# Optimization experiments

Measured on AMD Instinct MI355X. Metric: run time of the kernel, lower is better.

Reference implementation:

```python
import jax, jax.numpy as jnp
import numpy as np

B, U1, U2 = 4, 2048, 2048
C = 256      # in_feat_dim
F = 256      # feat_dim
M = 4        # num_modes
D = C // M   # attention_mode_dim = 64
ATTN_CLIP = 500.0
LN_EPS = 1e-12


def setup_inputs() -> dict:
    key = jax.random.key(0)
    ks = jax.random.split(key, 8)
    s = 0.02  # base_initializer_range
    inp = {
        "query_feat": jax.random.normal(ks[0], (B, U1, C), jnp.float32),
        "key_feat": jax.random.normal(ks[1], (B, U2, C), jnp.float32),
        "Wq": jax.random.normal(ks[2], (M * D, C), jnp.float32) * s,
        "bq": jnp.zeros((M * D,), jnp.float32),
    }
    # tie_qk_scheme='shared': key linear shares query weights
    inp["Wk"] = inp["Wq"]
    inp["bk"] = inp["bq"]
    inp["Wv"] = jax.random.normal(ks[3], (M * F, C), jnp.float32) * s  # first_linear, v_has_bias=False
    inp["W_mid"] = jax.random.normal(ks[4], (F, F), jnp.float32) * s   # MMSharedMid shared_linear
    inp["b_mid"] = jnp.zeros((F,), jnp.float32)
    inp["W_out"] = jax.random.normal(ks[5], (M, F, F), jnp.float32) * s  # grouped 1x1 conv, per mode
    inp["b_out"] = jnp.zeros((M, F), jnp.float32)
    inp["ln_g"] = jnp.ones((F,), jnp.float32)   # resout LayerNorm
    inp["ln_b"] = jnp.zeros((F,), jnp.float32)
    inp["W_score"] = jax.random.normal(ks[6], (1, F), jnp.float32) * s  # LearnedSoftAggregate
    inp["b_score"] = jnp.zeros((1,), jnp.float32)
    return inp


def _layer_norm(x, g, b):
    mu = jnp.mean(x, axis=-1, keepdims=True)
    var = jnp.var(x, axis=-1, keepdims=True)
    return (x - mu) * jax.lax.rsqrt(var + LN_EPS) * g + b


def reference(query_feat, key_feat, Wq, bq, Wk, bk, Wv, W_mid, b_mid,
              W_out, b_out, ln_g, ln_b, W_score, b_score):
    # --- tied-QK multi-mode attention ---
    q = (query_feat @ Wq.T + bq).reshape(B, U1, M, D)
    k = (key_feat @ Wk.T + bk).reshape(B, U2, M, D)
    scores = jnp.einsum('bimd,bjmd->bmij', q, k) / jnp.sqrt(jnp.float32(D))
    scores = jnp.clip(scores, -ATTN_CLIP, ATTN_CLIP)  # attn_clip
    probs = jax.nn.softmax(scores, axis=-1)           # [B, M, U1, U2]

    # --- ExpandedFeatTrans: value projection + fusion ---
    v = (key_feat @ Wv.T).reshape(B, U2, M, F)        # first_linear (no bias)
    fused = jnp.einsum('bmij,bjmf->bmif', probs, v)   # [B, M, U1, F]

    # MMSharedMid: shared linear over F + gelu (dropout = identity in eval)
    mid = jax.nn.gelu(fused @ W_mid.T + b_mid, approximate=False)

    # MMPrivateOutput: per-mode grouped 1x1 conv; NOTE the original code computes
    # x_comb = x + shortcut but then layer-norms x (shortcut dropped) - kept faithful.
    out = jnp.einsum('bmif,mgf->bmig', mid, W_out) + b_out[None, :, None, :]
    out = _layer_norm(out, ln_g, ln_b)                # [B, M, U1, F]

    # LearnedSoftAggregate over modes (group_dim=1, keepdim=False)
    mode_scores = out @ W_score.T + b_score           # [B, M, U1, 1]
    mode_probs = jax.nn.softmax(mode_scores, axis=1)
    return jnp.sum(out * mode_probs, axis=1)          # [B, U1, F]
```

## Files before the change

kernel.cpp:

```cpp
#include <hip/hip_runtime.h>

typedef __attribute__((ext_vector_type(8))) short short8;
typedef __attribute__((ext_vector_type(4))) float f32x4;
typedef __attribute__((ext_vector_type(16))) float f32x16;
typedef unsigned short u16t;
typedef unsigned int u32t;

#define MFMA16(a, b, c) __builtin_amdgcn_mfma_f32_16x16x32_bf16((a), (b), (c), 0, 0, 0)
#define MFMA32(a, b, c) __builtin_amdgcn_mfma_f32_32x32x16_bf16((a), (b), (c), 0, 0, 0)

__device__ __forceinline__ u16t f2bf(float f) {
  u32t u = __float_as_uint(f);
  u32t r = u + 0x7fffu + ((u >> 16) & 1u);
  return (u16t)(r >> 16);
}
__device__ __forceinline__ float bf2f(u16t b) {
  return __uint_as_float(((u32t)b) << 16);
}
__device__ __forceinline__ short8 pack8(float4 a0, float4 a1) {
  short8 r;
  r[0] = (short)f2bf(a0.x); r[1] = (short)f2bf(a0.y);
  r[2] = (short)f2bf(a0.z); r[3] = (short)f2bf(a0.w);
  r[4] = (short)f2bf(a1.x); r[5] = (short)f2bf(a1.y);
  r[6] = (short)f2bf(a1.z); r[7] = (short)f2bf(a1.w);
  return r;
}
__device__ __forceinline__ u32t packrhu(float a, float b) {
  u32t ua = __float_as_uint(a) + 0x8000u;
  u32t ub = __float_as_uint(b) + 0x8000u;
  return (ua >> 16) | (ub & 0xffff0000u);
}

__global__ __launch_bounds__(256) void cvt_kernel(
    const float* __restrict__ Wq, const float* __restrict__ Wv,
    const float* __restrict__ Wm, const float* __restrict__ Wo,
    u16t* __restrict__ WqB, u16t* __restrict__ WvB,
    u16t* __restrict__ WmB, u16t* __restrict__ WoB) {
  const int blk = blockIdx.x, tid = threadIdx.x;
  const float* src; u16t* dst; int base;
  if (blk < 64)       { src = Wq; dst = WqB; base = blk * 1024; }
  else if (blk < 320) { src = Wv; dst = WvB; base = (blk - 64) * 1024; }
  else if (blk < 384) { src = Wm; dst = WmB; base = (blk - 320) * 1024; }
  else                { src = Wo; dst = WoB; base = (blk - 384) * 1024; }
  int i = base + tid * 4;
  float4 v = *(const float4*)(src + i);
  ushort4 o;
  o.x = f2bf(v.x); o.y = f2bf(v.y); o.z = f2bf(v.z); o.w = f2bf(v.w);
  *(ushort4*)(dst + i) = o;
}

__global__ __launch_bounds__(256, 4) void proj_kernel(
    const float* __restrict__ query, const float* __restrict__ key,
    const u16t* __restrict__ WqB, const u16t* __restrict__ WvB,
    const float* __restrict__ bq,
    u16t* __restrict__ QfB, u16t* __restrict__ KfB, u16t* __restrict__ VfB) {
  __shared__ __align__(16) u16t Cs[64 * 72];
  const int tid = threadIdx.x;
  const int w = tid >> 6, lane = tid & 63, quad = lane >> 4, l15 = lane & 15;
  const int l31 = lane & 31, h8 = (lane >> 5) * 8;
  const int wrow = (w >> 1) * 32, wcol = (w & 1) * 32;

  const float* A; const u16t* W16; const float* bias;
  float ascale; u16t* out; int mode, bx, byg;
  const int blk = blockIdx.x;
  if (blk < 128) {
    A = query; W16 = WqB; bias = bq; ascale = 0.125f; out = QfB; mode = 0; bx = blk; byg = 0;
  } else if (blk < 256) {
    A = key; W16 = WqB; bias = bq; ascale = 1.0f; out = KfB; mode = 0; bx = blk - 128; byg = 0;
  } else {
    int v2 = blk - 256;
    A = key; W16 = WvB; bias = nullptr; ascale = 1.0f; out = VfB; mode = 1;
    bx = v2 & 127; byg = v2 >> 7;
  }
  const int rt = bx * 64;

  const f32x4 fz = {0.f, 0.f, 0.f, 0.f};
  f32x4 acc[4][2][2];
#pragma unroll
  for (int n = 0; n < 4; n++)
#pragma unroll
    for (int i = 0; i < 2; i++)
#pragma unroll
      for (int j = 0; j < 2; j++) acc[n][i][j] = fz;

  const float* arow0 = A + (size_t)(rt + wrow + l15) * 256;
  const float* arow1 = A + (size_t)(rt + wrow + 16 + l15) * 256;
  const u16t* wbase = W16 + (size_t)(byg * 256 + wcol + l15) * 256;

#pragma unroll
  for (int ks = 0; ks < 8; ++ks) {
    const int kk = ks * 32 + quad * 8;
    float4 a00 = *(const float4*)(arow0 + kk);
    float4 a01 = *(const float4*)(arow0 + kk + 4);
    float4 a10 = *(const float4*)(arow1 + kk);
    float4 a11 = *(const float4*)(arow1 + kk + 4);
    a00.x *= ascale; a00.y *= ascale; a00.z *= ascale; a00.w *= ascale;
    a01.x *= ascale; a01.y *= ascale; a01.z *= ascale; a01.w *= ascale;
    a10.x *= ascale; a10.y *= ascale; a10.z *= ascale; a10.w *= ascale;
    a11.x *= ascale; a11.y *= ascale; a11.z *= ascale; a11.w *= ascale;
    short8 af0 = pack8(a00, a01);
    short8 af1 = pack8(a10, a11);
#pragma unroll
    for (int nby = 0; nby < 4; ++nby) {
      const u16t* wb = wbase + (size_t)nby * 64 * 256 + kk;
      short8 bw0 = *(const short8*)(wb);
      short8 bw1 = *(const short8*)(wb + 16 * 256);
      acc[nby][0][0] = MFMA16(af0, bw0, acc[nby][0][0]);
      acc[nby][0][1] = MFMA16(af0, bw1, acc[nby][0][1]);
      acc[nby][1][0] = MFMA16(af1, bw0, acc[nby][1][0]);
      acc[nby][1][1] = MFMA16(af1, bw1, acc[nby][1][1]);
    }
  }

#pragma unroll 1
  for (int nby = 0; nby < 4; ++nby) {
    const int by = byg * 4 + nby;
    const int ct = by * 64;
    __syncthreads();
    if (mode == 0) {
#pragma unroll
      for (int i = 0; i < 2; i++) {
        int rl = wrow + i * 16 + quad * 4;
#pragma unroll
        for (int j = 0; j < 2; j++) {
          int cl = wcol + j * 16 + l15;
          float bv = bias ? bias[ct + cl] * ascale : 0.f;
#pragma unroll
          for (int rg = 0; rg < 4; ++rg)
            Cs[(rl + rg) * 72 + cl] = f2bf(acc[nby][i][j][rg] + bv);
        }
      }
    } else {
#pragma unroll
      for (int i = 0; i < 2; i++) {
        int rl = wrow + i * 16 + quad * 4;
#pragma unroll
        for (int j = 0; j < 2; j++) {
          int cl = wcol + j * 16 + l15;
          ushort4 pk;
          pk.x = f2bf(acc[nby][i][j][0]);
          pk.y = f2bf(acc[nby][i][j][1]);
          pk.z = f2bf(acc[nby][i][j][2]);
          pk.w = f2bf(acc[nby][i][j][3]);
          *(ushort4*)&Cs[cl * 72 + rl] = pk;
        }
      }
    }
    __syncthreads();
#pragma unroll
    for (int t2 = 0; t2 < 2; ++t2) {
      short8 frag = *(const short8*)&Cs[(t2 * 32 + l31) * 72 + w * 16 + h8];
      size_t base;
      if (mode == 0) {
        int b = rt >> 11, m = by;
        int it32 = ((rt & 2047) >> 5) + t2;
        base = (((size_t)(b * 4 + m) * 64 + it32) * 4 + w) * 512;
      } else {
        int b = rt >> 11, m = by >> 2;
        int fb = ((by & 3) << 1) + t2;
        int jt16 = ((rt & 2047) >> 4) + w;
        base = (((size_t)(b * 4 + m) * 8 + fb) * 128 + jt16) * 512;
      }
      *(short8*)(out + base + lane * 8) = frag;
    }
  }
}

__global__ __launch_bounds__(256, 4) void attn_kernel(
    const u16t* __restrict__ Qf, const u16t* __restrict__ Kf,
    const u16t* __restrict__ Vf,
    const u16t* __restrict__ Wmid, const u16t* __restrict__ Wout,
    const float* __restrict__ b_mid, const float* __restrict__ b_out,
    const float* __restrict__ ln_g, const float* __restrict__ ln_b,
    const float* __restrict__ Wsc, const float* __restrict__ b_sc,
    u16t* __restrict__ out_ln, float* __restrict__ scoresWS) {
  __shared__ __align__(16) u16t smF[32 * 264];
  __shared__ __align__(16) u16t smP[2][32 * 132];
  __shared__ float smL[128];
  __shared__ float smR[128];
  __shared__ float smS[64];
  const int tid = threadIdx.x;
  const int w = tid >> 6, lane = tid & 63, quad = lane >> 4, l15 = lane & 15;
  const int l31 = lane & 31, h = lane >> 5;
  const int L = blockIdx.x;
  const int xcd = L & 7, slot = L >> 3;
  const int bm = xcd * 2 + (slot >> 6);
  const int it32 = slot & 63;
  const int m = bm & 3;
  const int q0 = it32 * 32;

  const size_t lane8 = (size_t)lane * 8;

  const u16t* qbase = Qf + ((size_t)(bm * 64 + it32) * 4) * 512 + lane8;
  short8 qf4[4];
#pragma unroll
  for (int ksd = 0; ksd < 4; ++ksd)
    qf4[ksd] = *(const short8*)(qbase + ksd * 512);

  const u16t* kbase = Kf + ((size_t)bm * 256) * 512 + lane8;
  const u16t* vbase = Vf + ((size_t)(bm * 8 + 2 * w) * 128) * 512 + lane8;

  f32x16 facc[2];
#pragma unroll
  for (int j = 0; j < 2; j++)
#pragma unroll
    for (int r = 0; r < 16; r++) facc[j][r] = 0.f;
  float lsum = 0.f;

  short8 kf4[4];
#pragma unroll
  for (int ksd = 0; ksd < 4; ++ksd)
    kf4[ksd] = *(const short8*)(kbase + (size_t)w * 2048 + ksd * 512);

  {
    f32x16 sacc;
#pragma unroll
    for (int r = 0; r < 16; r++) sacc[r] = 0.f;
#pragma unroll
    for (int ksd = 0; ksd < 4; ++ksd)
      sacc = MFMA32(kf4[ksd], qf4[ksd], sacc);
    float ls = 0.f;
#pragma unroll
    for (int tt = 0; tt < 8; ++tt) {
      const int jl = ((2 * tt) & 3) + 8 * ((2 * tt) >> 2) + 4 * h;
      float p0 = __expf(sacc[2 * tt]);
      float p1 = __expf(sacc[2 * tt + 1]);
      ls += p0 + p1;
      *(u32t*)&smP[0][l31 * 132 + w * 32 + jl] = packrhu(p0, p1);
    }
    lsum += ls;
  }
#pragma unroll
  for (int ksd = 0; ksd < 4; ++ksd)
    kf4[ksd] = *(const short8*)(kbase + (size_t)(4 + w) * 2048 + ksd * 512);
  __syncthreads();

#pragma unroll 1
  for (int t = 0; t < 16; ++t) {
    u16t* Pb = &smP[t & 1][0];
    u16t* Pn = &smP[(t + 1) & 1][0];

    if (t < 15) {
      f32x16 sacc;
#pragma unroll
      for (int r = 0; r < 16; r++) sacc[r] = 0.f;
#pragma unroll
      for (int ksd = 0; ksd < 4; ++ksd)
        sacc = MFMA32(kf4[ksd], qf4[ksd], sacc);
      float ls = 0.f;
#pragma unroll
      for (int tt = 0; tt < 8; ++tt) {
        const int jl = ((2 * tt) & 3) + 8 * ((2 * tt) >> 2) + 4 * h;
        float p0 = __expf(sacc[2 * tt]);
        float p1 = __expf(sacc[2 * tt + 1]);
        ls += p0 + p1;
        *(u32t*)&Pn[l31 * 132 + w * 32 + jl] = packrhu(p0, p1);
      }
      lsum += ls;
    }
    if (t < 14) {
      const int jn = (t + 2) * 4 + w;
#pragma unroll
      for (int ksd = 0; ksd < 4; ++ksd)
        kf4[ksd] = *(const short8*)(kbase + (size_t)jn * 2048 + ksd * 512);
    }
#pragma unroll
    for (int jj = 0; jj < 4; ++jj) {
      short8 vf[2][2];
#pragma unroll
      for (int fb = 0; fb < 2; ++fb)
#pragma unroll
        for (int ks2 = 0; ks2 < 2; ++ks2)
          vf[fb][ks2] = *(const short8*)(vbase + ((size_t)fb * 128 + (t * 8 + jj * 2 + ks2)) * 512);
      short8 bbL[2];
#pragma unroll
      for (int ks2 = 0; ks2 < 2; ++ks2)
        bbL[ks2] = *(const short8*)&Pb[l31 * 132 + jj * 32 + ks2 * 16 + h * 8];
      facc[0] = MFMA32(vf[0][0], bbL[0], facc[0]);
      facc[0] = MFMA32(vf[0][1], bbL[1], facc[0]);
      facc[1] = MFMA32(vf[1][0], bbL[0], facc[1]);
      facc[1] = MFMA32(vf[1][1], bbL[1], facc[1]);
    }
    __syncthreads();
  }

  lsum += __shfl_xor(lsum, 32);
  if (h == 0) smL[w * 32 + l31] = lsum;
  __syncthreads();
  float inv = 1.f / (smL[l31] + smL[32 + l31] + smL[64 + l31] + smL[96 + l31]);

#pragma unroll
  for (int fb = 0; fb < 2; ++fb) {
#pragma unroll
    for (int g = 0; g < 4; ++g) {
      int fbase = w * 64 + fb * 32 + 8 * g + 4 * h;
      ushort4 pk4;
      pk4.x = f2bf(facc[fb][4 * g + 0] * inv);
      pk4.y = f2bf(facc[fb][4 * g + 1] * inv);
      pk4.z = f2bf(facc[fb][4 * g + 2] * inv);
      pk4.w = f2bf(facc[fb][4 * g + 3] * inv);
      *(ushort4*)&smF[l31 * 264 + fbase] = pk4;
    }
  }
  __syncthreads();

  const int rgrp = w >> 1, ch = w & 1;
  const int rowq = rgrp * 16 + quad * 4;
  const f32x4 fz4 = {0.f, 0.f, 0.f, 0.f};

  f32x4 macc[8];
#pragma unroll
  for (int i = 0; i < 8; i++) macc[i] = fz4;
  for (int kc = 0; kc < 8; ++kc) {
    short8 af = *(const short8*)&smF[(rgrp * 16 + l15) * 264 + kc * 32 + quad * 8];
#pragma unroll
    for (int nb = 0; nb < 8; ++nb) {
      short8 bw = *(const short8*)(Wmid + (size_t)(ch * 128 + nb * 16 + l15) * 256 + kc * 32 + quad * 8);
      macc[nb] = MFMA16(af, bw, macc[nb]);
    }
  }
#pragma unroll
  for (int nb = 0; nb < 8; ++nb) {
    int c = ch * 128 + nb * 16 + l15;
    float bmv = b_mid[c];
#pragma unroll
    for (int rg = 0; rg < 4; ++rg) {
      float x = macc[nb][rg] + bmv;
      macc[nb][rg] = 0.5f * x * (1.f + erff(x * 0.70710678118654752f));
    }
  }
  __syncthreads();
#pragma unroll
  for (int nb = 0; nb < 8; ++nb)
#pragma unroll
    for (int rg = 0; rg < 4; ++rg)
      smF[(rowq + rg) * 264 + ch * 128 + nb * 16 + l15] = f2bf(macc[nb][rg]);
  __syncthreads();

  const u16t* Wo = Wout + (size_t)m * 65536;
  f32x4 oacc[8];
#pragma unroll
  for (int i = 0; i < 8; i++) oacc[i] = fz4;
  for (int kc = 0; kc < 8; ++kc) {
    short8 af = *(const short8*)&smF[(rgrp * 16 + l15) * 264 + kc * 32 + quad * 8];
#pragma unroll
    for (int nb = 0; nb < 8; ++nb) {
      short8 bw = *(const short8*)(Wo + (size_t)(ch * 128 + nb * 16 + l15) * 256 + kc * 32 + quad * 8);
      oacc[nb] = MFMA16(af, bw, oacc[nb]);
    }
  }

  float sum[4] = {0, 0, 0, 0}, sq[4] = {0, 0, 0, 0};
#pragma unroll
  for (int nb = 0; nb < 8; ++nb) {
    int c = ch * 128 + nb * 16 + l15;
    float bo = b_out[m * 256 + c];
#pragma unroll
    for (int rg = 0; rg < 4; ++rg) {
      float x = oacc[nb][rg] + bo;
      oacc[nb][rg] = x;
      sum[rg] += x;
      sq[rg] += x * x;
    }
  }
#pragma unroll
  for (int rg = 0; rg < 4; ++rg) {
    float s = sum[rg], s2 = sq[rg];
    s += __shfl_xor(s, 1); s += __shfl_xor(s, 2); s += __shfl_xor(s, 4); s += __shfl_xor(s, 8);
    s2 += __shfl_xor(s2, 1); s2 += __shfl_xor(s2, 2); s2 += __shfl_xor(s2, 4); s2 += __shfl_xor(s2, 8);
    if (l15 == 0) {
      smR[(rowq + rg) + 32 * ch] = s;
      smR[64 + (rowq + rg) + 32 * ch] = s2;
    }
  }
  __syncthreads();
  float mu[4], rstd[4];
#pragma unroll
  for (int rg = 0; rg < 4; ++rg) {
    int r = rowq + rg;
    float s = smR[r] + smR[r + 32];
    float s2 = smR[64 + r] + smR[64 + r + 32];
    float mean = s * (1.f / 256.f);
    float var = s2 * (1.f / 256.f) - mean * mean;
    mu[rg] = mean;
    rstd[rg] = rsqrtf(var + 1e-12f);
  }

  float scp[4] = {0, 0, 0, 0};
#pragma unroll
  for (int nb = 0; nb < 8; ++nb) {
    int c = ch * 128 + nb * 16 + l15;
    float g = ln_g[c], bb2 = ln_b[c], wsv = Wsc[c];
#pragma unroll
    for (int rg = 0; rg < 4; ++rg) {
      float xn = (oacc[nb][rg] - mu[rg]) * rstd[rg] * g + bb2;
      out_ln[((size_t)bm * 2048 + (q0 + rowq + rg)) * 256 + c] = f2bf(xn);
      scp[rg] += xn * wsv;
    }
  }
#pragma unroll
  for (int rg = 0; rg < 4; ++rg) {
    float s = scp[rg];
    s += __shfl_xor(s, 1); s += __shfl_xor(s, 2); s += __shfl_xor(s, 4); s += __shfl_xor(s, 8);
    if (l15 == 0) smS[(rowq + rg) + 32 * ch] = s;
  }
  __syncthreads();
  if (ch == 0 && l15 == 0) {
#pragma unroll
    for (int rg = 0; rg < 4; ++rg) {
      int r = rowq + rg;
      scoresWS[bm * 2048 + q0 + r] = smS[r] + smS[r + 32] + b_sc[0];
    }
  }
}

__global__ __launch_bounds__(256) void agg_kernel(
    const u16t* __restrict__ out_ln, const float* __restrict__ scoresWS,
    float* __restrict__ out) {
  const int row = blockIdx.x;
  const int c = threadIdx.x;
  const int b = row >> 11, i = row & 2047;
  float s0 = scoresWS[(b * 4 + 0) * 2048 + i];
  float s1 = scoresWS[(b * 4 + 1) * 2048 + i];
  float s2 = scoresWS[(b * 4 + 2) * 2048 + i];
  float s3 = scoresWS[(b * 4 + 3) * 2048 + i];
  float mx = fmaxf(fmaxf(s0, s1), fmaxf(s2, s3));
  float e0 = __expf(s0 - mx), e1 = __expf(s1 - mx), e2 = __expf(s2 - mx), e3 = __expf(s3 - mx);
  float inv = 1.f / (e0 + e1 + e2 + e3);
  float acc = e0 * inv * bf2f(out_ln[((size_t)(b * 4 + 0) * 2048 + i) * 256 + c]) +
              e1 * inv * bf2f(out_ln[((size_t)(b * 4 + 1) * 2048 + i) * 256 + c]) +
              e2 * inv * bf2f(out_ln[((size_t)(b * 4 + 2) * 2048 + i) * 256 + c]) +
              e3 * inv * bf2f(out_ln[((size_t)(b * 4 + 3) * 2048 + i) * 256 + c]);
  out[(size_t)row * 256 + c] = acc;
}

extern "C" void kernel_launch(void* const* d_in, const int* in_sizes, int n_in,
                              void* d_out, int out_size, void* d_ws, size_t ws_size,
                              hipStream_t stream) {
  (void)in_sizes; (void)n_in; (void)out_size; (void)ws_size;
  const float* query = (const float*)d_in[0];
  const float* key   = (const float*)d_in[1];
  const float* Wq    = (const float*)d_in[2];
  const float* bq    = (const float*)d_in[3];
  const float* Wv    = (const float*)d_in[6];
  const float* Wm    = (const float*)d_in[7];
  const float* bmid  = (const float*)d_in[8];
  const float* Wo    = (const float*)d_in[9];
  const float* bo    = (const float*)d_in[10];
  const float* lng   = (const float*)d_in[11];
  const float* lnb   = (const float*)d_in[12];
  const float* Wsc   = (const float*)d_in[13];
  const float* bsc   = (const float*)d_in[14];

  char* p = (char*)d_ws;
  u16t* QfB = (u16t*)p; p += (size_t)2097152 * 2;
  u16t* KfB = (u16t*)p; p += (size_t)2097152 * 2;
  u16t* VfB = (u16t*)p; p += (size_t)8388608 * 2;
  u16t* WmB = (u16t*)p; p += (size_t)65536 * 2;
  u16t* WoB = (u16t*)p; p += (size_t)262144 * 2;
  u16t* WqB = (u16t*)p; p += (size_t)65536 * 2;
  u16t* WvB = (u16t*)p; p += (size_t)262144 * 2;
  u16t* outLn = (u16t*)p; p += (size_t)8388608 * 2;
  float* scWS = (float*)p; p += (size_t)32768 * 4;

  cvt_kernel<<<640, 256, 0, stream>>>(Wq, Wv, Wm, Wo, WqB, WvB, WmB, WoB);

  proj_kernel<<<768, 256, 0, stream>>>(query, key, WqB, WvB, bq,
                                       QfB, KfB, VfB);

  attn_kernel<<<1024, 256, 0, stream>>>(QfB, KfB, VfB, WmB, WoB,
                                        bmid, bo, lng, lnb, Wsc, bsc,
                                        outLn, scWS);

  agg_kernel<<<8192, 256, 0, stream>>>(outLn, scWS, (float*)d_out);
}
```

Before: 277.7 us.

## Reuse key A-fragments across K and V tiles; prefetch V fragments in attention

The projection kernel now loads and converts each 64-row block of the input once into register fragments. It then loops over several output column tiles, K and V together for key blocks, which halves the grid and avoids re-reading and re-packing key_feat for the separate K and V blocks. In the attention kernel, all 16 V fragments for a tile are issued as loads at the top of each iteration, ahead of the score MFMAs, so their latency overlaps compute. The occupancy hint is lowered to 3 waves per SIMD to make room for the extra registers. The trade-offs are more registers per thread, lower occupancy, and fewer, longer-running projection blocks.

```diff
diff --git a/kernel.cpp b/kernel.cpp
--- a/kernel.cpp
+++ b/kernel.cpp
@@ -49,7 +49,7 @@
   *(ushort4*)(dst + i) = o;
 }
 
-__global__ __launch_bounds__(256, 4) void proj_kernel(
+__global__ __launch_bounds__(256) void proj_kernel(
     const float* __restrict__ query, const float* __restrict__ key,
     const u16t* __restrict__ WqB, const u16t* __restrict__ WvB,
     const float* __restrict__ bq,
@@ -60,62 +60,69 @@
   const int l31 = lane & 31, h8 = (lane >> 5) * 8;
   const int wrow = (w >> 1) * 32, wcol = (w & 1) * 32;
 
-  const float* A; const u16t* W16; const float* bias;
-  float ascale; u16t* out; int mode, bx, byg;
   const int blk = blockIdx.x;
+  const float* A; float ascale; int bx, nK, nV, kby0, vby0;
+  u16t* out0;
   if (blk < 128) {
-    A = query; W16 = WqB; bias = bq; ascale = 0.125f; out = QfB; mode = 0; bx = blk; byg = 0;
-  } else if (blk < 256) {
-    A = key; W16 = WqB; bias = bq; ascale = 1.0f; out = KfB; mode = 0; bx = blk - 128; byg = 0;
+    A = query; ascale = 0.125f; bx = blk; nK = 4; nV = 0; kby0 = 0; vby0 = 0;
+    out0 = QfB;
   } else {
-    int v2 = blk - 256;
-    A = key; W16 = WvB; bias = nullptr; ascale = 1.0f; out = VfB; mode = 1;
-    bx = v2 & 127; byg = v2 >> 7;
+    int kb = blk - 128;
+    bx = kb & 127; int byg = kb >> 7;
+    A = key; ascale = 1.0f; nK = 2; nV = 8; kby0 = byg * 2; vby0 = byg * 8;
+    out0 = KfB;
   }
   const int rt = bx * 64;
 
-  const f32x4 fz = {0.f, 0.f, 0.f, 0.f};
-  f32x4 acc[4][2][2];
-#pragma unroll
-  for (int n = 0; n < 4; n++)
+  short8 af[8][2];
+  {
+    const float* arow0 = A + (size_t)(rt + wrow + l15) * 256;
+    const float* arow1 = arow0 + 16 * 256;
+#pragma unroll
+    for (int ks = 0; ks < 8; ++ks) {
+      const int kk = ks * 32 + quad * 8;
+      float4 a00 = *(const float4*)(arow0 + kk);
+      float4 a01 = *(const float4*)(arow0 + kk + 4);
+      float4 a10 = *(const float4*)(arow1 + kk);
+      float4 a11 = *(const float4*)(arow1 + kk + 4);
+      a00.x *= ascale; a00.y *= ascale; a00.z *= ascale; a00.w *= ascale;
+      a01.x *= ascale; a01.y *= ascale; a01.z *= ascale; a01.w *= ascale;
+      a10.x *= ascale; a10.y *= ascale; a10.z *= ascale; a10.w *= ascale;
+      a11.x *= ascale; a11.y *= ascale; a11.z *= ascale; a11.w *= ascale;
+      af[ks][0] = pack8(a00, a01);
+      af[ks][1] = pack8(a10, a11);
+    }
+  }
+
+  const int ntiles = nK + nV;
+#pragma unroll 1
+  for (int tix = 0; tix < ntiles; ++tix) {
+    const bool isK = tix < nK;
+    const int by = isK ? (kby0 + tix) : (vby0 + (tix - nK));
+    const u16t* W16 = isK ? WqB : WvB;
+    u16t* outp = isK ? out0 : VfB;
+    const int mode = isK ? 0 : 1;
+    const int ct = by * 64;
+
+    const f32x4 fz = {0.f, 0.f, 0.f, 0.f};
+    f32x4 acc[2][2];
 #pragma unroll
     for (int i = 0; i < 2; i++)
 #pragma unroll
-      for (int j = 0; j < 2; j++) acc[n][i][j] = fz;
-
-  const float* arow0 = A + (size_t)(rt + wrow + l15) * 256;
-  const float* arow1 = A + (size_t)(rt + wrow + 16 + l15) * 256;
-  const u16t* wbase = W16 + (size_t)(byg * 256 + wcol + l15) * 256;
-
-#pragma unroll
-  for (int ks = 0; ks < 8; ++ks) {
-    const int kk = ks * 32 + quad * 8;
-    float4 a00 = *(const float4*)(arow0 + kk);
-    float4 a01 = *(const float4*)(arow0 + kk + 4);
-    float4 a10 = *(const float4*)(arow1 + kk);
-    float4 a11 = *(const float4*)(arow1 + kk + 4);
-    a00.x *= ascale; a00.y *= ascale; a00.z *= ascale; a00.w *= ascale;
-    a01.x *= ascale; a01.y *= ascale; a01.z *= ascale; a01.w *= ascale;
-    a10.x *= ascale; a10.y *= ascale; a10.z *= ascale; a10.w *= ascale;
-    a11.x *= ascale; a11.y *= ascale; a11.z *= ascale; a11.w *= ascale;
-    short8 af0 = pack8(a00, a01);
-    short8 af1 = pack8(a10, a11);
-#pragma unroll
-    for (int nby = 0; nby < 4; ++nby) {
-      const u16t* wb = wbase + (size_t)nby * 64 * 256 + kk;
-      short8 bw0 = *(const short8*)(wb);
-      short8 bw1 = *(const short8*)(wb + 16 * 256);
-      acc[nby][0][0] = MFMA16(af0, bw0, acc[nby][0][0]);
-      acc[nby][0][1] = MFMA16(af0, bw1, acc[nby][0][1]);
-      acc[nby][1][0] = MFMA16(af1, bw0, acc[nby][1][0]);
-      acc[nby][1][1] = MFMA16(af1, bw1, acc[nby][1][1]);
-    }
-  }
-
-#pragma unroll 1
-  for (int nby = 0; nby < 4; ++nby) {
-    const int by = byg * 4 + nby;
-    const int ct = by * 64;
+      for (int j = 0; j < 2; j++) acc[i][j] = fz;
+
+    const u16t* wb0 = W16 + (size_t)(ct + wcol + l15) * 256;
+#pragma unroll
+    for (int ks = 0; ks < 8; ++ks) {
+      const int kk = ks * 32 + quad * 8;
+      short8 bw0 = *(const short8*)(wb0 + kk);
+      short8 bw1 = *(const short8*)(wb0 + 16 * 256 + kk);
+      acc[0][0] = MFMA16(af[ks][0], bw0, acc[0][0]);
+      acc[0][1] = MFMA16(af[ks][0], bw1, acc[0][1]);
+      acc[1][0] = MFMA16(af[ks][1], bw0, acc[1][0]);
+      acc[1][1] = MFMA16(af[ks][1], bw1, acc[1][1]);
+    }
+
     __syncthreads();
     if (mode == 0) {
 #pragma unroll
@@ -124,10 +131,10 @@
 #pragma unroll
         for (int j = 0; j < 2; j++) {
           int cl = wcol + j * 16 + l15;
-          float bv = bias ? bias[ct + cl] * ascale : 0.f;
+          float bv = bq[ct + cl] * ascale;
 #pragma unroll
           for (int rg = 0; rg < 4; ++rg)
-            Cs[(rl + rg) * 72 + cl] = f2bf(acc[nby][i][j][rg] + bv);
+            Cs[(rl + rg) * 72 + cl] = f2bf(acc[i][j][rg] + bv);
         }
       }
     } else {
@@ -138,10 +145,10 @@
         for (int j = 0; j < 2; j++) {
           int cl = wcol + j * 16 + l15;
           ushort4 pk;
-          pk.x = f2bf(acc[nby][i][j][0]);
-          pk.y = f2bf(acc[nby][i][j][1]);
-          pk.z = f2bf(acc[nby][i][j][2]);
-          pk.w = f2bf(acc[nby][i][j][3]);
+          pk.x = f2bf(acc[i][j][0]);
+          pk.y = f2bf(acc[i][j][1]);
+          pk.z = f2bf(acc[i][j][2]);
+          pk.w = f2bf(acc[i][j][3]);
           *(ushort4*)&Cs[cl * 72 + rl] = pk;
         }
       }
@@ -161,12 +168,12 @@
         int jt16 = ((rt & 2047) >> 4) + w;
         base = (((size_t)(b * 4 + m) * 8 + fb) * 128 + jt16) * 512;
       }
-      *(short8*)(out + base + lane * 8) = frag;
-    }
-  }
-}
-
-__global__ __launch_bounds__(256, 4) void attn_kernel(
+      *(short8*)(outp + base + lane * 8) = frag;
+    }
+  }
+}
+
+__global__ __launch_bounds__(256, 3) void attn_kernel(
     const u16t* __restrict__ Qf, const u16t* __restrict__ Kf,
     const u16t* __restrict__ Vf,
     const u16t* __restrict__ Wmid, const u16t* __restrict__ Wout,
@@ -240,6 +247,11 @@
     u16t* Pb = &smP[t & 1][0];
     u16t* Pn = &smP[(t + 1) & 1][0];
 
+    short8 vf[16];
+#pragma unroll
+    for (int u = 0; u < 16; ++u)
+      vf[u] = *(const short8*)(vbase + ((size_t)(u >> 3) * 128 + (t * 8 + (u & 7))) * 512);
+
     if (t < 15) {
       f32x16 sacc;
 #pragma unroll
@@ -266,20 +278,12 @@
     }
 #pragma unroll
     for (int jj = 0; jj < 4; ++jj) {
-      short8 vf[2][2];
-#pragma unroll
-      for (int fb = 0; fb < 2; ++fb)
-#pragma unroll
-        for (int ks2 = 0; ks2 < 2; ++ks2)
-          vf[fb][ks2] = *(const short8*)(vbase + ((size_t)fb * 128 + (t * 8 + jj * 2 + ks2)) * 512);
-      short8 bbL[2];
-#pragma unroll
-      for (int ks2 = 0; ks2 < 2; ++ks2)
-        bbL[ks2] = *(const short8*)&Pb[l31 * 132 + jj * 32 + ks2 * 16 + h * 8];
-      facc[0] = MFMA32(vf[0][0], bbL[0], facc[0]);
-      facc[0] = MFMA32(vf[0][1], bbL[1], facc[0]);
-      facc[1] = MFMA32(vf[1][0], bbL[0], facc[1]);
-      facc[1] = MFMA32(vf[1][1], bbL[1], facc[1]);
+      short8 b0 = *(const short8*)&Pb[l31 * 132 + jj * 32 + h * 8];
+      short8 b1 = *(const short8*)&Pb[l31 * 132 + jj * 32 + 16 + h * 8];
+      facc[0] = MFMA32(vf[jj * 2], b0, facc[0]);
+      facc[0] = MFMA32(vf[jj * 2 + 1], b1, facc[0]);
+      facc[1] = MFMA32(vf[8 + jj * 2], b0, facc[1]);
+      facc[1] = MFMA32(vf[8 + jj * 2 + 1], b1, facc[1]);
     }
     __syncthreads();
   }
@@ -465,7 +469,7 @@
 
   cvt_kernel<<<640, 256, 0, stream>>>(Wq, Wv, Wm, Wo, WqB, WvB, WmB, WoB);
 
-  proj_kernel<<<768, 256, 0, stream>>>(query, key, WqB, WvB, bq,
+  proj_kernel<<<384, 256, 0, stream>>>(query, key, WqB, WvB, bq,
                                        QfB, KfB, VfB);
 
   attn_kernel<<<1024, 256, 0, stream>>>(QfB, KfB, VfB, WmB, WoB,
```

Result: faster. 270.8 us (-2.5%).
